# Kernel tuning notes

Hardware: AMD Instinct MI355X
Metric: run time of the kernel (lower is better)

## Reference

```python
import jax, jax.numpy as jnp
import numpy as np

B, N, K, OUT = 8, 4096, 30, 13


def _knn(x, k):
    # x: [N, C]; k nearest neighbors by squared L2 (self included, as in PyG knn)
    s = jnp.sum(x * x, axis=-1)
    d = s[:, None] + s[None, :] - 2.0 * (x @ x.T)  # [N, N]
    return jax.lax.top_k(-d, k)[1]  # [N, k]


def _edge_conv(x, w1, b1, w2, b2, k):
    # DynamicEdgeConv: dynamic kNN graph on x, edge MLP on [x_i, x_j - x_i], max aggr.
    idx = jax.vmap(lambda xb: _knn(xb, k))(jax.lax.stop_gradient(x))  # [B, N, k]
    xj = jax.vmap(lambda xb, ib: xb[ib])(x, idx)  # [B, N, k, C]
    xi = x[:, :, None, :]
    e = jnp.concatenate([jnp.broadcast_to(xi, xj.shape), xj - xi], axis=-1)  # [B,N,k,2C]
    h = jax.nn.relu(e @ w1 + b1)  # MLP([2C, 64, 64]); BN treated as identity (eval)
    h = h @ w2 + b2  # plain last layer (PyG MLP plain_last=True)
    return jnp.max(h, axis=2)  # max aggregation over neighbors -> [B, N, 64]


def setup_inputs() -> dict:
    key = jax.random.key(0)
    ks = jax.random.split(key, 16)

    def w(kk, shape):
        return (jax.random.normal(kk, shape, jnp.float32) / np.sqrt(shape[0])).astype(jnp.float32)

    inp = {"points": jax.random.normal(ks[0], (B, N, 6), jnp.float32)}
    i = 1
    for name, ci, co in [("c1", 12, 64), ("c2", 128, 64), ("c3", 128, 64)]:
        inp[name + "w1"] = w(ks[i], (ci, co)); inp[name + "b1"] = jnp.zeros((co,), jnp.float32); i += 1
        inp[name + "w2"] = w(ks[i], (co, co)); inp[name + "b2"] = jnp.zeros((co,), jnp.float32); i += 1
    for j, (ci, co) in enumerate([(192, 1024), (1024, 256), (256, 128), (128, OUT)], 1):
        inp["mw%d" % j] = w(ks[i], (ci, co)); inp["mb%d" % j] = jnp.zeros((co,), jnp.float32); i += 1
    return inp


def reference(points, c1w1, c1b1, c1w2, c1b2, c2w1, c2b1, c2w2, c2b2,
              c3w1, c3b1, c3w2, c3b2, mw1, mb1, mw2, mb2, mw3, mb3, mw4, mb4):
    x1 = _edge_conv(points, c1w1, c1b1, c1w2, c1b2, K)
    x2 = _edge_conv(x1, c2w1, c2b1, c2w2, c2b2, K)
    x3 = _edge_conv(x2, c3w1, c3b1, c3w2, c3b2, K)
    h = jnp.concatenate([x1, x2, x3], axis=-1).reshape(B * N, 192)
    h = jax.nn.relu(h @ mw1 + mb1)  # dropout is identity in eval
    h = jax.nn.relu(h @ mw2 + mb2)
    h = jax.nn.relu(h @ mw3 + mb3)
    out = h @ mw4 + mb4
    return jax.nn.log_softmax(out, axis=1)
```

## Files before the change

### kernel.cpp

```cpp
#include <hip/hip_runtime.h>
#include <math.h>

#define NPTS 4096
#define NBATCH 8
#define TOTAL (NBATCH*NPTS)
#define KNN 30

__device__ __forceinline__ unsigned key_xform(float v) {
  unsigned u = __float_as_uint(v);
  return (u & 0x80000000u) ? ~u : (u | 0x80000000u);
}
__device__ __forceinline__ float key_unxform(unsigned k) {
  unsigned u = (k & 0x80000000u) ? (k ^ 0x80000000u) : ~k;
  return __uint_as_float(u);
}

__global__ void norms_k(const float* __restrict__ X, int rs, int C, float* __restrict__ S) {
  int i = blockIdx.x * 256 + threadIdx.x;
  if (i >= TOTAL) return;
  const float* r = X + (size_t)i * rs;
  float a = 0.f;
  if ((C & 3) == 0) {
    for (int c4 = 0; c4 < (C >> 2); ++c4) {
      float4 v = *(const float4*)(r + c4 * 4);
      a = fmaf(v.x, v.x, a); a = fmaf(v.y, v.y, a);
      a = fmaf(v.z, v.z, a); a = fmaf(v.w, v.w, a);
    }
  } else {
    for (int c = 0; c < C; ++c) { float v = r[c]; a = fmaf(v, v, a); }
  }
  S[i] = a;
}

__global__ __launch_bounds__(256) void dist_k(const float* __restrict__ X, int rs, int C,
    const float* __restrict__ S, int rowBase, float* __restrict__ D) {
  __shared__ __align__(16) float At[64][128];
  __shared__ __align__(16) float Bt[64][128];
  __shared__ float sA[128], sB[128];
  int tid = threadIdx.x;
  int bx = blockIdx.x, by = blockIdx.y;
  int gr0 = rowBase + by * 128;
  int batch0 = gr0 >> 12;
  int a0 = gr0;
  int b0 = (batch0 << 12) + bx * 128;
  if (tid < 128) sA[tid] = S[a0 + tid];
  else           sB[tid - 128] = S[b0 + tid - 128];
  if ((C & 3) == 0) {
    int nv = 128 * (C >> 2);
    for (int i = tid; i < nv; i += 256) {
      int m = i & 127, kq = i >> 7;
      float4 va = *(const float4*)(X + (size_t)(a0 + m) * rs + kq * 4);
      At[kq*4+0][m] = va.x; At[kq*4+1][m] = va.y; At[kq*4+2][m] = va.z; At[kq*4+3][m] = va.w;
      float4 vb = *(const float4*)(X + (size_t)(b0 + m) * rs + kq * 4);
      Bt[kq*4+0][m] = vb.x; Bt[kq*4+1][m] = vb.y; Bt[kq*4+2][m] = vb.z; Bt[kq*4+3][m] = vb.w;
    }
  } else {
    for (int i = tid; i < 128 * C; i += 256) {
      int m = i & 127, k = i >> 7;
      At[k][m] = X[(size_t)(a0 + m) * rs + k];
      Bt[k][m] = X[(size_t)(b0 + m) * rs + k];
    }
  }
  __syncthreads();
  float acc[8][8] = {};
  int tx = tid & 15, ty = tid >> 4;
  for (int k = 0; k < C; ++k) {
    float av[8], bv[8];
    *(float4*)&av[0] = *(const float4*)&At[k][ty * 4];
    *(float4*)&av[4] = *(const float4*)&At[k][ty * 4 + 64];
    *(float4*)&bv[0] = *(const float4*)&Bt[k][tx * 4];
    *(float4*)&bv[4] = *(const float4*)&Bt[k][tx * 4 + 64];
#pragma unroll
    for (int i = 0; i < 8; ++i)
#pragma unroll
      for (int j = 0; j < 8; ++j) acc[i][j] = fmaf(av[i], bv[j], acc[i][j]);
  }
#pragma unroll
  for (int ih = 0; ih < 2; ++ih)
#pragma unroll
  for (int i2 = 0; i2 < 4; ++i2) {
    int i = ih * 4 + i2;
    int row = ty * 4 + i2 + ih * 64;
    int lr = by * 128 + row;
    float si = sA[row];
#pragma unroll
    for (int jh = 0; jh < 2; ++jh) {
      int cb = jh * 64 + tx * 4;
      float4 o;
      o.x = si + sB[cb+0] - 2.f * acc[i][jh*4+0];
      o.y = si + sB[cb+1] - 2.f * acc[i][jh*4+1];
      o.z = si + sB[cb+2] - 2.f * acc[i][jh*4+2];
      o.w = si + sB[cb+3] - 2.f * acc[i][jh*4+3];
      *(float4*)(D + (size_t)lr * NPTS + bx * 128 + cb) = o;
    }
  }
}

#define SENTK 0xFFFFFFFFFFFFFFFFull
__global__ __launch_bounds__(64) void topk_k(const float* __restrict__ D, int* __restrict__ IDXo,
                                             int rowBase) {
  int lane = threadIdx.x;
  int gr = rowBase + blockIdx.x;
  int bBase = gr & ~(NPTS - 1);
  const float* drow = D + (size_t)blockIdx.x * NPTS;
  float4 dv[16];
#pragma unroll
  for (int q = 0; q < 16; ++q) dv[q] = ((const float4*)drow)[lane + 64 * q];
  unsigned long long k1 = SENTK, k2 = SENTK;
#pragma unroll
  for (int q = 0; q < 16; ++q) {
#pragma unroll
    for (int r = 0; r < 4; ++r) {
      float d = (r == 0) ? dv[q].x : (r == 1) ? dv[q].y : (r == 2) ? dv[q].z : dv[q].w;
      unsigned idx = 4u * (lane + 64u * q) + r;
      unsigned long long kk = ((unsigned long long)key_xform(d) << 32) | idx;
      if (kk < k1) { k2 = k1; k1 = kk; } else if (kk < k2) k2 = kk;
    }
  }
  for (int it = 0; it < KNN; ++it) {
    unsigned long long km = k1;
#pragma unroll
    for (int d = 1; d < 64; d <<= 1) {
      unsigned long long o = __shfl_xor(km, d);
      if (o < km) km = o;
    }
    unsigned widx = (unsigned)(km & 0xFFFFFFFFu);
    if (lane == 0) IDXo[(size_t)gr * KNN + it] = bBase + (int)widx;
    if (((widx >> 2) & 63u) == (unsigned)lane) {
      if (k2 != SENTK) { k1 = k2; k2 = SENTK; }
      else {
        k1 = SENTK; k2 = SENTK;
#pragma unroll
        for (int q = 0; q < 16; ++q) {
#pragma unroll
          for (int r = 0; r < 4; ++r) {
            float d = (r == 0) ? dv[q].x : (r == 1) ? dv[q].y : (r == 2) ? dv[q].z : dv[q].w;
            unsigned idx = 4u * (lane + 64u * q) + r;
            unsigned long long kk = ((unsigned long long)key_xform(d) << 32) | idx;
            if (kk > km) {
              if (kk < k1) { k2 = k1; k1 = kk; } else if (kk < k2) k2 = kk;
            }
          }
        }
      }
    }
  }
}

__global__ __launch_bounds__(256) void uv_k(const float* __restrict__ X, int rs, int C,
    const float* __restrict__ W1, const float* __restrict__ B1,
    float* __restrict__ U, float* __restrict__ V) {
  __shared__ float wd[64][64];
  __shared__ float wb[64][64];
  __shared__ float xs[4][64];
  int tid = threadIdx.x;
  int c = tid & 63, pl = tid >> 6;
  for (int i = tid; i < C * 64; i += 256) {
    float a = W1[i], b = W1[C * 64 + i];
    wd[i >> 6][i & 63] = a - b;
    wb[i >> 6][i & 63] = b;
  }
  int p0 = blockIdx.x * 4;
  for (int i = tid; i < 4 * C; i += 256)
    xs[i / C][i % C] = X[(size_t)(p0 + i / C) * rs + (i % C)];
  __syncthreads();
  float u = B1[c], v = 0.f;
  for (int k = 0; k < C; ++k) {
    float x = xs[pl][k];
    u = fmaf(x, wd[k][c], u);
    v = fmaf(x, wb[k][c], v);
  }
  int p = p0 + pl;
  U[(size_t)p * 64 + c] = u;
  V[(size_t)p * 64 + c] = v;
}

__global__ __launch_bounds__(256) void edge_k(const float* __restrict__ U, const float* __restrict__ V,
    const float* __restrict__ W2, const float* __restrict__ B2, const int* __restrict__ IDX,
    float* __restrict__ F, int colOut) {
  __shared__ __align__(16) float At[16][260];
  __shared__ __align__(16) float W2s[64][64];
  __shared__ __align__(16) float us[8][64];
  __shared__ int idxs[256];
  __shared__ unsigned om[512];
  int tid = threadIdx.x;
  int p0 = blockIdx.x * 8;
  for (int i = tid; i < 1024; i += 256) ((float4*)W2s)[i] = ((const float4*)W2)[i];
  for (int i = tid; i < 128; i += 256)
    ((float4*)us)[i] = ((const float4*)(U + (size_t)p0 * 64))[i];
  for (int m = tid; m < 256; m += 256)
    idxs[m] = IDX[(size_t)p0 * KNN + (m < 240 ? m : 239)];
  for (int i = tid; i < 512; i += 256) om[i] = 0u;
  __syncthreads();
  float acc[8][8] = {};
  int tx = tid & 7, ty = tid >> 3;
  for (int kc = 0; kc < 4; ++kc) {
    for (int i = tid; i < 1024; i += 256) {
      int m = i >> 2, kq = i & 3;
      int um = m / 30; if (um > 7) um = 7;
      float4 vv = *(const float4*)(V + (size_t)idxs[m] * 64 + kc * 16 + kq * 4);
      float4 uu = *(const float4*)&us[um][kc * 16 + kq * 4];
      At[kq*4+0][m] = fmaxf(uu.x + vv.x, 0.f);
      At[kq*4+1][m] = fmaxf(uu.y + vv.y, 0.f);
      At[kq*4+2][m] = fmaxf(uu.z + vv.z, 0.f);
      At[kq*4+3][m] = fmaxf(uu.w + vv.w, 0.f);
    }
    __syncthreads();
#pragma unroll
    for (int k = 0; k < 16; ++k) {
      float av[8], bv[8];
      *(float4*)&av[0] = *(const float4*)&At[k][ty * 4];
      *(float4*)&av[4] = *(const float4*)&At[k][ty * 4 + 128];
      *(float4*)&bv[0] = *(const float4*)&W2s[kc * 16 + k][tx * 4];
      *(float4*)&bv[4] = *(const float4*)&W2s[kc * 16 + k][tx * 4 + 32];
#pragma unroll
      for (int i = 0; i < 8; ++i)
#pragma unroll
        for (int j = 0; j < 8; ++j) acc[i][j] = fmaf(av[i], bv[j], acc[i][j]);
    }
    __syncthreads();
  }
#pragma unroll
  for (int ih = 0; ih < 2; ++ih) {
    int mbase = ty * 4 + ih * 128;
    if (mbase >= 240) continue;
    int ptA = mbase / 30;
    int ptB = (mbase + 3) / 30;
    int split = (ptB > ptA) ? (ptB * 30 - mbase) : 4;
    float mx[8];
#pragma unroll
    for (int j = 0; j < 8; ++j) mx[j] = acc[ih*4+0][j];
#pragma unroll
    for (int i2 = 1; i2 < 4; ++i2) {
      bool flushNow = (i2 == split);
      if (flushNow) {
#pragma unroll
        for (int j = 0; j < 8; ++j)
          atomicMax(&om[ptA * 64 + tx * 4 + (j & 3) + (j >> 2) * 32], key_xform(mx[j]));
#pragma unroll
        for (int j = 0; j < 8; ++j) mx[j] = acc[ih*4+i2][j];
      } else {
#pragma unroll
        for (int j = 0; j < 8; ++j) mx[j] = fmaxf(mx[j], acc[ih*4+i2][j]);
      }
    }
    int ptEnd = (split == 4) ? ptA : ptB;
#pragma unroll
    for (int j = 0; j < 8; ++j)
      atomicMax(&om[ptEnd * 64 + tx * 4 + (j & 3) + (j >> 2) * 32], key_xform(mx[j]));
  }
  __syncthreads();
  for (int i = tid; i < 512; i += 256) {
    int pt = i >> 6, c = i & 63;
    F[(size_t)(p0 + pt) * 192 + colOut + c] = key_unxform(om[i]) + B2[c];
  }
}

__global__ __launch_bounds__(256) void gemm_k(const float* __restrict__ A, const float* __restrict__ B,
    const float* __restrict__ bias, float* __restrict__ C, int M, int N, int Kd, int lda, int doRelu) {
  __shared__ __align__(16) float At[16][128];
  __shared__ __align__(16) float Bs[16][128];
  int tid = threadIdx.x, bx = blockIdx.x, by = blockIdx.y;
  int m0 = by * 128, n0 = bx * 128;
  float acc[8][8] = {};
  int tx = tid & 15, ty = tid >> 4;
  for (int k0 = 0; k0 < Kd; k0 += 16) {
    if (k0) __syncthreads();
    for (int i = tid; i < 512; i += 256) {
      int m = i & 127, kq = i >> 7;
      float4 v = *(const float4*)(A + (size_t)(m0 + m) * lda + k0 + kq * 4);
      At[kq*4+0][m] = v.x; At[kq*4+1][m] = v.y; At[kq*4+2][m] = v.z; At[kq*4+3][m] = v.w;
    }
    for (int i = tid; i < 512; i += 256) {
      int n4 = i & 31, k = i >> 5;
      *(float4*)&Bs[k][n4 * 4] = *(const float4*)(B + (size_t)(k0 + k) * N + n0 + n4 * 4);
    }
    __syncthreads();
#pragma unroll
    for (int k = 0; k < 16; ++k) {
      float av[8], bv[8];
      *(float4*)&av[0] = *(const float4*)&At[k][ty * 4];
      *(float4*)&av[4] = *(const float4*)&At[k][ty * 4 + 64];
      *(float4*)&bv[0] = *(const float4*)&Bs[k][tx * 4];
      *(float4*)&bv[4] = *(const float4*)&Bs[k][tx * 4 + 64];
#pragma unroll
      for (int i = 0; i < 8; ++i)
#pragma unroll
        for (int j = 0; j < 8; ++j) acc[i][j] = fmaf(av[i], bv[j], acc[i][j]);
    }
  }
#pragma unroll
  for (int ih = 0; ih < 2; ++ih)
#pragma unroll
  for (int i2 = 0; i2 < 4; ++i2) {
    int i = ih * 4 + i2;
    int m = m0 + ty * 4 + i2 + ih * 64;
#pragma unroll
    for (int jh = 0; jh < 2; ++jh) {
      int cb = n0 + jh * 64 + tx * 4;
      float o[4];
#pragma unroll
      for (int j2 = 0; j2 < 4; ++j2) {
        float x = acc[i][jh*4+j2] + bias[cb + j2];
        o[j2] = doRelu ? fmaxf(x, 0.f) : x;
      }
      *(float4*)(C + (size_t)m * N + cb) = *(float4*)&o[0];
    }
  }
}

__global__ __launch_bounds__(256) void final_k(const float* __restrict__ H, const float* __restrict__ W4,
                        const float* __restrict__ B4, float* __restrict__ O, int rows) {
  __shared__ float w4s[128 * 13];
  __shared__ float b4s[13];
  int tid = threadIdx.x;
  for (int i = tid; i < 1664; i += 256) w4s[i] = W4[i];
  if (tid < 13) b4s[tid] = B4[tid];
  __syncthreads();
  int r = blockIdx.x * 256 + tid;
  if (r >= rows) return;
  const float* h = H + (size_t)r * 128;
  float l[13];
#pragma unroll
  for (int c = 0; c < 13; ++c) l[c] = b4s[c];
  for (int k4 = 0; k4 < 32; ++k4) {
    float4 hv = *(const float4*)(h + k4 * 4);
#pragma unroll
    for (int q = 0; q < 4; ++q) {
      float x = (q == 0) ? hv.x : (q == 1) ? hv.y : (q == 2) ? hv.z : hv.w;
      int k = k4 * 4 + q;
#pragma unroll
      for (int c = 0; c < 13; ++c) l[c] = fmaf(x, w4s[k * 13 + c], l[c]);
    }
  }
  float mx = l[0];
#pragma unroll
  for (int c = 1; c < 13; ++c) mx = fmaxf(mx, l[c]);
  float s = 0.f;
#pragma unroll
  for (int c = 0; c < 13; ++c) s += expf(l[c] - mx);
  float lse = mx + logf(s);
  float* op = O + (size_t)r * 13;
#pragma unroll
  for (int c = 0; c < 13; ++c) op[c] = l[c] - lse;
}

extern "C" void kernel_launch(void* const* d_in, const int* in_sizes, int n_in,
                              void* d_out, int out_size, void* d_ws, size_t ws_size,
                              hipStream_t stream) {
  const float* P = (const float*)d_in[0];
  const float* W1s[3] = {(const float*)d_in[1], (const float*)d_in[5], (const float*)d_in[9]};
  const float* B1s[3] = {(const float*)d_in[2], (const float*)d_in[6], (const float*)d_in[10]};
  const float* W2s_[3] = {(const float*)d_in[3], (const float*)d_in[7], (const float*)d_in[11]};
  const float* B2s[3] = {(const float*)d_in[4], (const float*)d_in[8], (const float*)d_in[12]};
  const float* MW1 = (const float*)d_in[13]; const float* MB1 = (const float*)d_in[14];
  const float* MW2 = (const float*)d_in[15]; const float* MB2 = (const float*)d_in[16];
  const float* MW3 = (const float*)d_in[17]; const float* MB3 = (const float*)d_in[18];
  const float* MW4 = (const float*)d_in[19]; const float* MB4 = (const float*)d_in[20];

  char* w = (char*)d_ws;
  float* F   = (float*)(w + 0);
  float* S   = (float*)(w + 25165824);
  float* U   = (float*)(w + 25296896);
  float* V   = (float*)(w + 33685504);
  int*   IDX = (int*)  (w + 42074112);
  float* D   = (float*)(w + 46006272);
  (void)in_sizes; (void)n_in; (void)out_size;

  bool bigWS = (ws_size >= 213778432u);

  for (int l = 0; l < 3; ++l) {
    const float* X = (l == 0) ? P : (F + (l - 1) * 64);
    int rs = (l == 0) ? 6 : 192;
    int C  = (l == 0) ? 6 : 64;
    norms_k<<<TOTAL / 256, 256, 0, stream>>>(X, rs, C, S);
    if (bigWS) {
      for (int g = 0; g < 4; ++g) {
        dist_k<<<dim3(32, 64), 256, 0, stream>>>(X, rs, C, S, g * 8192, D);
        topk_k<<<8192, 64, 0, stream>>>(D, IDX, g * 8192);
      }
    } else {
      for (int g = 0; g < 16; ++g) {
        dist_k<<<dim3(32, 16), 256, 0, stream>>>(X, rs, C, S, g * 2048, D);
        topk_k<<<2048, 64, 0, stream>>>(D, IDX, g * 2048);
      }
    }
    uv_k<<<TOTAL / 4, 256, 0, stream>>>(X, rs, C, W1s[l], B1s[l], U, V);
    edge_k<<<TOTAL / 8, 256, 0, stream>>>(U, V, W2s_[l], B2s[l], IDX, F, l * 64);
  }

  float* OUT = (float*)d_out;
  if (bigWS) {
    float* T1 = (float*)(w + 46006272);
    float* T2 = (float*)(w + 180224000);
    float* T3 = (float*)(w + 25296896);
    gemm_k<<<dim3(8, 256), 256, 0, stream>>>(F, MW1, MB1, T1, 32768, 1024, 192, 192, 1);
    gemm_k<<<dim3(2, 256), 256, 0, stream>>>(T1, MW2, MB2, T2, 32768, 256, 1024, 1024, 1);
    gemm_k<<<dim3(1, 256), 256, 0, stream>>>(T2, MW3, MB3, T3, 32768, 128, 256, 256, 1);
    final_k<<<128, 256, 0, stream>>>(T3, MW4, MB4, OUT, 32768);
  } else {
    float* T1 = D;
    float* T2 = U;
    float* T3 = V;
    for (int ch = 0; ch < 4; ++ch) {
      const float* A0 = F + (size_t)ch * 8192 * 192;
      gemm_k<<<dim3(8, 64), 256, 0, stream>>>(A0, MW1, MB1, T1, 8192, 1024, 192, 192, 1);
      gemm_k<<<dim3(2, 64), 256, 0, stream>>>(T1, MW2, MB2, T2, 8192, 256, 1024, 1024, 1);
      gemm_k<<<dim3(1, 64), 256, 0, stream>>>(T2, MW3, MB3, T3, 8192, 128, 256, 256, 1);
      final_k<<<8192 / 256, 256, 0, stream>>>(T3, MW4, MB4, OUT + (size_t)ch * 8192 * 13, 8192);
    }
  }
}
```

Baseline: 3.234 ms.

## Use split-bf16 MFMA GEMMs for the head MLP layers

Replaces the fp32 SIMT GEMMs in the classifier head with an MFMA kernel. It emulates fp32 precision by splitting A and B into high and low bf16 parts and running three products per tile (hh, hl, lh). Weights are pre-packed each call into an MFMA-friendly tiled layout, and activations are converted on the fly while staging to shared memory. This targets the FLOP-heavy 192→1024→256→128 GEMMs, at the cost of extra packing kernels, conversion work and a slightly lower precision than true fp32. It applies only to the big-workspace path.

```diff
diff --git a/kernel.cpp b/kernel.cpp
--- a/kernel.cpp
+++ b/kernel.cpp
@@ -6,6 +6,9 @@
 #define TOTAL (NBATCH*NPTS)
 #define KNN 30
 
+typedef __attribute__((ext_vector_type(8))) __bf16 bf16x8;
+typedef __attribute__((ext_vector_type(4))) float f32x4;
+
 __device__ __forceinline__ unsigned key_xform(float v) {
   unsigned u = __float_as_uint(v);
   return (u & 0x80000000u) ? ~u : (u | 0x80000000u);
@@ -13,6 +16,10 @@
 __device__ __forceinline__ float key_unxform(unsigned k) {
   unsigned u = (k & 0x80000000u) ? (k ^ 0x80000000u) : ~k;
   return __uint_as_float(u);
+}
+__device__ __forceinline__ unsigned short bf16_rne(float x) {
+  unsigned u = __float_as_uint(x);
+  return (unsigned short)((u + 0x7FFFu + ((u >> 16) & 1u)) >> 16);
 }
 
 __global__ void norms_k(const float* __restrict__ X, int rs, int C, float* __restrict__ S) {
@@ -309,6 +316,91 @@
   }
 }
 
+__global__ void packw_k(const float* __restrict__ W, int Kd, int N,
+                        unsigned short* __restrict__ Ph, unsigned short* __restrict__ Pl) {
+  int i = blockIdx.x * 256 + threadIdx.x;
+  if (i >= Kd * N) return;
+  int k = i / N, n = i % N;
+  float w = W[i];
+  unsigned short hb = bf16_rne(w);
+  unsigned short lb = bf16_rne(w - __uint_as_float((unsigned)hb << 16));
+  size_t dst = ((size_t)(n >> 4) * (Kd >> 3) + (k >> 3)) * 128 + (size_t)(n & 15) * 8 + (k & 7);
+  Ph[dst] = hb; Pl[dst] = lb;
+}
+
+__global__ __launch_bounds__(256) void gemm_mfma_k(const float* __restrict__ A,
+    const unsigned short* __restrict__ Bh, const unsigned short* __restrict__ Bl,
+    const float* __restrict__ bias, float* __restrict__ C,
+    int N, int Kd, int lda, int doRelu) {
+  __shared__ __align__(16) unsigned short Ash[4096], Asl[4096], Bsh[4096], Bsl[4096];
+  int tid = threadIdx.x;
+  int bx = blockIdx.x, by = blockIdx.y;
+  int m0 = by * 128, n0 = bx * 128;
+  int wid = tid >> 6, lane = tid & 63;
+  int mw = (wid >> 1) * 64, nw = (wid & 1) * 64;
+  int Kb = Kd >> 3;
+  f32x4 acc[4][4] = {};
+  for (int k0 = 0; k0 < Kd; k0 += 32) {
+    if (k0) __syncthreads();
+    for (int s = tid; s < 1024; s += 256) {
+      int m = s >> 3, q = s & 7;
+      float4 v = *(const float4*)(A + (size_t)(m0 + m) * lda + k0 + q * 4);
+      unsigned short h0 = bf16_rne(v.x), h1 = bf16_rne(v.y), h2 = bf16_rne(v.z), h3 = bf16_rne(v.w);
+      unsigned short l0 = bf16_rne(v.x - __uint_as_float((unsigned)h0 << 16));
+      unsigned short l1 = bf16_rne(v.y - __uint_as_float((unsigned)h1 << 16));
+      unsigned short l2 = bf16_rne(v.z - __uint_as_float((unsigned)h2 << 16));
+      unsigned short l3 = bf16_rne(v.w - __uint_as_float((unsigned)h3 << 16));
+      int eo = (((m >> 4) * 4 + (q >> 1)) * 16 + (m & 15)) * 8 + (q & 1) * 4;
+      ushort4 hv; hv.x = h0; hv.y = h1; hv.z = h2; hv.w = h3;
+      ushort4 lv; lv.x = l0; lv.y = l1; lv.z = l2; lv.w = l3;
+      *(ushort4*)(Ash + eo) = hv;
+      *(ushort4*)(Asl + eo) = lv;
+    }
+    for (int s = tid; s < 1024; s += 256) {
+      int p = s >> 9, r = s & 511;
+      int nt = r >> 6, kk = r & 63;
+      int kg = kk >> 4, u = kk & 15;
+      size_t src = ((size_t)((n0 >> 4) + nt) * Kb + (k0 >> 3) + kg) * 16 + u;
+      uint4 val = p ? ((const uint4*)Bl)[src] : ((const uint4*)Bh)[src];
+      ((uint4*)(p ? Bsl : Bsh))[(nt * 4 + kg) * 16 + u] = val;
+    }
+    __syncthreads();
+    bf16x8 ah[4], al[4], bhf[4], blf[4];
+#pragma unroll
+    for (int t = 0; t < 4; ++t) {
+      int ao = ((mw >> 4) + t) * 1024 + lane * 16;
+      int bo = ((nw >> 4) + t) * 1024 + lane * 16;
+      ah[t]  = *(const bf16x8*)((const char*)Ash + ao);
+      al[t]  = *(const bf16x8*)((const char*)Asl + ao);
+      bhf[t] = *(const bf16x8*)((const char*)Bsh + bo);
+      blf[t] = *(const bf16x8*)((const char*)Bsl + bo);
+    }
+#pragma unroll
+    for (int mt = 0; mt < 4; ++mt)
+#pragma unroll
+      for (int nt = 0; nt < 4; ++nt) {
+        acc[mt][nt] = __builtin_amdgcn_mfma_f32_16x16x32_bf16(ah[mt], bhf[nt], acc[mt][nt], 0, 0, 0);
+        acc[mt][nt] = __builtin_amdgcn_mfma_f32_16x16x32_bf16(ah[mt], blf[nt], acc[mt][nt], 0, 0, 0);
+        acc[mt][nt] = __builtin_amdgcn_mfma_f32_16x16x32_bf16(al[mt], bhf[nt], acc[mt][nt], 0, 0, 0);
+      }
+  }
+#pragma unroll
+  for (int nt = 0; nt < 4; ++nt) {
+    int col = n0 + nw + nt * 16 + (lane & 15);
+    float b = bias[col];
+#pragma unroll
+    for (int mt = 0; mt < 4; ++mt) {
+      int rbase = m0 + mw + mt * 16 + ((lane >> 4) << 2);
+#pragma unroll
+      for (int r = 0; r < 4; ++r) {
+        float x = acc[mt][nt][r] + b;
+        if (doRelu) x = fmaxf(x, 0.f);
+        C[(size_t)(rbase + r) * N + col] = x;
+      }
+    }
+  }
+}
+
 __global__ __launch_bounds__(256) void final_k(const float* __restrict__ H, const float* __restrict__ W4,
                         const float* __restrict__ B4, float* __restrict__ O, int rows) {
   __shared__ float w4s[128 * 13];
@@ -394,9 +486,18 @@
     float* T1 = (float*)(w + 46006272);
     float* T2 = (float*)(w + 180224000);
     float* T3 = (float*)(w + 25296896);
-    gemm_k<<<dim3(8, 256), 256, 0, stream>>>(F, MW1, MB1, T1, 32768, 1024, 192, 192, 1);
-    gemm_k<<<dim3(2, 256), 256, 0, stream>>>(T1, MW2, MB2, T2, 32768, 256, 1024, 1024, 1);
-    gemm_k<<<dim3(1, 256), 256, 0, stream>>>(T2, MW3, MB3, T3, 32768, 128, 256, 256, 1);
+    unsigned short* PW1h = (unsigned short*)(w + 42074112);
+    unsigned short* PW1l = (unsigned short*)(w + 42467328);
+    unsigned short* PW2h = (unsigned short*)(w + 42860544);
+    unsigned short* PW2l = (unsigned short*)(w + 43384832);
+    unsigned short* PW3h = (unsigned short*)(w + 43909120);
+    unsigned short* PW3l = (unsigned short*)(w + 43974656);
+    packw_k<<<(192 * 1024) / 256, 256, 0, stream>>>(MW1, 192, 1024, PW1h, PW1l);
+    packw_k<<<(1024 * 256) / 256, 256, 0, stream>>>(MW2, 1024, 256, PW2h, PW2l);
+    packw_k<<<(256 * 128) / 256, 256, 0, stream>>>(MW3, 256, 128, PW3h, PW3l);
+    gemm_mfma_k<<<dim3(8, 256), 256, 0, stream>>>(F,  PW1h, PW1l, MB1, T1, 1024, 192, 192, 1);
+    gemm_mfma_k<<<dim3(2, 256), 256, 0, stream>>>(T1, PW2h, PW2l, MB2, T2, 256, 1024, 1024, 1);
+    gemm_mfma_k<<<dim3(1, 256), 256, 0, stream>>>(T2, PW3h, PW3l, MB3, T3, 128, 256, 256, 1);
     final_k<<<128, 256, 0, stream>>>(T3, MW4, MB4, OUT, 32768);
   } else {
     float* T1 = D;
```

After: 3.027 ms. -6.4%, faster.
